# Kernel tuning notes

Hardware: AMD Instinct MI355X
Metric: run time of the kernel (lower is better)

## Reference

```python
import jax, jax.numpy as jnp
import numpy as np

D_MODEL = 1024
N_LAYER = 2
VOCAB = 50257
D_STATE = 64
D_CONV = 4
EXPAND = 2
HEADDIM = 64
D_INNER = EXPAND * D_MODEL            # 2048
NHEADS = D_INNER // HEADDIM           # 32
CONV_DIM = D_INNER + 2 * D_STATE      # x, B, C share the conv (ngroups=1)
D_PROJ = 2 * D_INNER + 2 * D_STATE + NHEADS  # z, xBC, dt
D_FF = 4 * D_MODEL
B, T = 1, 1024
EPS = 1e-5


def _layernorm(x, w):
    mu = jnp.mean(x, -1, keepdims=True)
    v = jnp.mean((x - mu) ** 2, -1, keepdims=True)
    return (x - mu) * jax.lax.rsqrt(v + EPS) * w


def _rmsnorm(x, w):
    return x * jax.lax.rsqrt(jnp.mean(x ** 2, -1, keepdims=True) + EPS) * w


def setup_inputs() -> dict:
    key = jax.random.key(0)
    ks = jax.random.split(key, 16)
    std = 0.02
    idx = jax.random.randint(ks[0], (B, T), 0, VOCAB)
    targets = jax.random.randint(ks[1], (B, T), 0, VOCAB)
    E = jax.random.normal(ks[2], (VOCAB, D_MODEL)) * std  # tied embedding / lm_head
    norm_w = jnp.ones((N_LAYER, D_MODEL))
    norm2_w = jnp.ones((N_LAYER, D_MODEL))
    norm_f_w = jnp.ones((D_MODEL,))
    in_proj_w = jax.random.normal(ks[3], (N_LAYER, D_PROJ, D_MODEL)) * std
    conv_w = jax.random.normal(ks[4], (N_LAYER, CONV_DIM, D_CONV)) / np.sqrt(D_CONV)
    conv_b = jnp.zeros((N_LAYER, CONV_DIM))
    dt = jnp.exp(jax.random.uniform(ks[5], (N_LAYER, NHEADS)) * (np.log(0.1) - np.log(1e-3)) + np.log(1e-3))
    dt_bias = dt + jnp.log(-jnp.expm1(-dt))  # inverse softplus
    A_log = jnp.log(jax.random.uniform(ks[6], (N_LAYER, NHEADS), minval=1.0, maxval=16.0))
    Dp = jnp.ones((N_LAYER, NHEADS))
    gnorm_w = jnp.ones((N_LAYER, D_INNER))
    out_proj_w = jax.random.normal(ks[7], (N_LAYER, D_MODEL, D_INNER)) * std / np.sqrt(2 * N_LAYER)
    fc1_w = jax.random.normal(ks[8], (N_LAYER, 2 * D_FF, D_MODEL)) * std
    fc2_w = jax.random.normal(ks[9], (N_LAYER, D_MODEL, D_FF)) * std / np.sqrt(2 * N_LAYER)
    return {"idx": idx, "targets": targets, "E": E, "norm_w": norm_w, "norm2_w": norm2_w,
            "in_proj_w": in_proj_w, "conv_w": conv_w, "conv_b": conv_b, "dt_bias": dt_bias,
            "A_log": A_log, "Dp": Dp, "gnorm_w": gnorm_w, "out_proj_w": out_proj_w,
            "fc1_w": fc1_w, "fc2_w": fc2_w, "norm_f_w": norm_f_w}


def _mamba2(x, Wi, cw, cb, dtb, Al, Dh, gw, Wo):
    b, l, _ = x.shape
    zxbcdt = x @ Wi.T  # [b,l,D_PROJ]
    z = zxbcdt[..., :D_INNER]
    xBC = zxbcdt[..., D_INNER:D_INNER + CONV_DIM]
    dt = zxbcdt[..., D_INNER + CONV_DIM:]  # [b,l,H]
    # depthwise causal conv1d over time
    xp = jnp.pad(xBC, ((0, 0), (D_CONV - 1, 0), (0, 0)))
    xBC = sum(xp[:, k:k + l, :] * cw[:, k] for k in range(D_CONV)) + cb
    xBC = jax.nn.silu(xBC)
    xs = xBC[..., :D_INNER].reshape(b, l, NHEADS, HEADDIM)
    Bm = xBC[..., D_INNER:D_INNER + D_STATE]  # [b,l,N] (ngroups=1)
    Cm = xBC[..., D_INNER + D_STATE:]
    dt = jax.nn.softplus(dt + dtb)            # [b,l,H]
    dA = jnp.exp(dt * (-jnp.exp(Al)))         # [b,l,H]
    tm = lambda a: jnp.moveaxis(a, 1, 0)      # time-major for scan

    def step(h, inp):
        dA_t, dt_t, x_t, B_t, C_t = inp
        h = dA_t[..., None, None] * h + jnp.einsum('bh,bhp,bn->bhpn', dt_t, x_t, B_t)
        return h, jnp.einsum('bhpn,bn->bhp', h, C_t)

    h0 = jnp.zeros((b, NHEADS, HEADDIM, D_STATE), x.dtype)
    _, ys = jax.lax.scan(step, h0, (tm(dA), tm(dt), tm(xs), tm(Bm), tm(Cm)))
    y = jnp.moveaxis(ys, 0, 1) + Dh[None, None, :, None] * xs  # skip term D*x
    y = y.reshape(b, l, D_INNER)
    y = _rmsnorm(y * jax.nn.silu(z), gw)  # gated RMSNorm
    return y @ Wo.T


def _gated_mlp(x, W1, W2):
    y = x @ W1.T
    y, g = jnp.split(y, 2, axis=-1)
    return (y * jax.nn.silu(g)) @ W2.T


def reference(idx, targets, E, norm_w, norm2_w, in_proj_w, conv_w, conv_b, dt_bias,
              A_log, Dp, gnorm_w, out_proj_w, fc1_w, fc2_w, norm_f_w):
    h = E[idx]  # [B,T,D]
    for i in range(N_LAYER):
        x = _layernorm(h, norm_w[i])
        x = _mamba2(x, in_proj_w[i], conv_w[i], conv_b[i], dt_bias[i], A_log[i],
                    Dp[i], gnorm_w[i], out_proj_w[i])
        res = x + h
        x = _layernorm(res, norm2_w[i])
        h = _gated_mlp(x, fc1_w[i], fc2_w[i]) + res
    h = _layernorm(h, norm_f_w)
    logits = h @ E.T  # tied lm_head
    logp = jax.nn.log_softmax(logits, axis=-1)
    nll = -jnp.take_along_axis(logp, targets[..., None], axis=-1)[..., 0]
    loss = jnp.mean(nll)  # no ignore_index=-1 entries present
    return logits, loss
```

## Files before the change

### kernel.cpp

```cpp
#include <hip/hip_runtime.h>
#include <cmath>

#define DMODEL  1024
#define DINNER  2048
#define NHEADS  32
#define CONVDIM 2176
#define DPROJ   4256
#define VOCAB   50257
#define NBLK_V  400
#define VOCABP  (NBLK_V * 128)
#define CLEN    16
#define NCHUNK  64

typedef float f32x4 __attribute__((ext_vector_type(4)));
typedef float f32x2 __attribute__((ext_vector_type(2)));
typedef unsigned short u16;
typedef u16 u16x4 __attribute__((ext_vector_type(4)));
typedef u16 u16x8 __attribute__((ext_vector_type(8)));
typedef __bf16 bf16x8 __attribute__((ext_vector_type(8)));

__device__ __forceinline__ u16 f2bf(float f) {
  unsigned u = __builtin_bit_cast(unsigned, f);
  u += 0x7FFFu + ((u >> 16) & 1u);
  return (u16)(u >> 16);
}
__device__ __forceinline__ float silu_f(float x) { return x / (1.f + expf(-x)); }

__device__ __forceinline__ void gload16(const u16* g, u16* l) {
  __builtin_amdgcn_global_load_lds(
      (const __attribute__((address_space(1))) void*)g,
      (__attribute__((address_space(3))) void*)l,
      16, 0, 0);
}

__global__ __launch_bounds__(256) void gemm_bf16(
    const u16* __restrict__ A, const u16* __restrict__ B,
    float* __restrict__ C, int N, int K, int kslice,
    float* __restrict__ lsepart, int swz, int nblk)
{
  __shared__ alignas(128) u16 As[128 * 64];
  __shared__ alignas(128) u16 Bs[128 * 64];
  const int tid = threadIdx.x;
  int m0, n0;
  if (swz) {
    int bid = blockIdx.x;
    m0 = ((bid >> 3) & 7) << 7;
    n0 = ((bid & 7) + ((bid >> 6) << 3)) << 7;
  } else {
    m0 = blockIdx.x << 7;
    n0 = blockIdx.y << 7;
  }
  const int lane = tid & 63, wid = tid >> 6;
  const int wm = (wid >> 1) << 6, wn = (wid & 1) << 6;
  const int lr = lane & 15, kg = lane >> 4;

  const int srow = wid * 8 + (lane >> 3);
  const int scol = ((lane & 7) ^ (lane >> 3)) << 3;
  const u16* gA = A + (size_t)(m0 + srow) * K + scol;
  const u16* gB = B + (size_t)(n0 + srow) * K + scol;

  f32x4 acc[4][4];
#pragma unroll
  for (int i = 0; i < 4; ++i)
#pragma unroll
    for (int j = 0; j < 4; ++j) acc[i][j] = (f32x4){0.f, 0.f, 0.f, 0.f};

  const int kb = blockIdx.z * kslice;
  const int ke = kb + kslice;
  for (int k0 = kb; k0 < ke; k0 += 64) {
#pragma unroll
    for (int i = 0; i < 4; ++i) {
      gload16(gA + k0 + (size_t)i * 32 * K, As + i * 2048 + wid * 512);
      gload16(gB + k0 + (size_t)i * 32 * K, Bs + i * 2048 + wid * 512);
    }
    __syncthreads();
#pragma unroll
    for (int kk = 0; kk < 2; ++kk) {
      bf16x8 af[4], bfr[4];
      const int cx = ((kk * 4 + kg) ^ (lr & 7)) << 3;
#pragma unroll
      for (int f = 0; f < 4; ++f) {
        af[f]  = *(const bf16x8*)&As[(wm + f * 16 + lr) * 64 + cx];
        bfr[f] = *(const bf16x8*)&Bs[(wn + f * 16 + lr) * 64 + cx];
      }
#pragma unroll
      for (int i = 0; i < 4; ++i)
#pragma unroll
        for (int j = 0; j < 4; ++j)
          acc[i][j] = __builtin_amdgcn_mfma_f32_16x16x32_bf16(af[i], bfr[j], acc[i][j], 0, 0, 0);
    }
    __syncthreads();
  }

  const int mr = (lane >> 4) << 2;
  const int nc = lane & 15;
  float* Cw = C + (gridDim.z > 1 ? (size_t)blockIdx.z * 1024 * N : 0);
#pragma unroll
  for (int i = 0; i < 4; ++i)
#pragma unroll
    for (int j = 0; j < 4; ++j) {
      int n = n0 + wn + j * 16 + nc;
      if (n < N) {
#pragma unroll
        for (int e = 0; e < 4; ++e)
          Cw[(size_t)(m0 + wm + i * 16 + mr + e) * N + n] = acc[i][j][e];
      }
    }

  if (lsepart) {
    float* Ls = (float*)As;
#pragma unroll
    for (int i = 0; i < 4; ++i)
#pragma unroll
      for (int e = 0; e < 4; ++e) {
        float pm = -1e30f;
#pragma unroll
        for (int j = 0; j < 4; ++j) {
          int n = n0 + wn + j * 16 + nc;
          if (n < N) pm = fmaxf(pm, acc[i][j][e]);
        }
        float ps = 0.f;
#pragma unroll
        for (int j = 0; j < 4; ++j) {
          int n = n0 + wn + j * 16 + nc;
          if (n < N) ps += expf(acc[i][j][e] - pm);
        }
#pragma unroll
        for (int o = 1; o < 16; o <<= 1) {
          float pm2 = __shfl_xor(pm, o), ps2 = __shfl_xor(ps, o);
          float M = fmaxf(pm, pm2);
          ps = ps * expf(pm - M) + ps2 * expf(pm2 - M);
          pm = M;
        }
        if (nc == 0) {
          int row = wm + i * 16 + mr + e;
          Ls[row * 4 + (wid & 1) * 2] = pm;
          Ls[row * 4 + (wid & 1) * 2 + 1] = ps;
        }
      }
    __syncthreads();
    if (tid < 128) {
      float pa = Ls[tid * 4], sa = Ls[tid * 4 + 1];
      float pb = Ls[tid * 4 + 2], sb = Ls[tid * 4 + 3];
      float M = fmaxf(pa, pb);
      float S = sa * expf(pa - M) + sb * expf(pb - M);
      ((f32x2*)lsepart)[(size_t)(m0 + tid) * nblk + (n0 >> 7)] = (f32x2){M, S};
    }
  }
}

__global__ void k_cvt8(const float* __restrict__ src, u16* __restrict__ dst, int n8) {
  int i = blockIdx.x * 256 + threadIdx.x;
  if (i >= n8) return;
  f32x4 a = ((const f32x4*)src)[i * 2];
  f32x4 b = ((const f32x4*)src)[i * 2 + 1];
  u16x8 o = { f2bf(a[0]), f2bf(a[1]), f2bf(a[2]), f2bf(a[3]),
              f2bf(b[0]), f2bf(b[1]), f2bf(b[2]), f2bf(b[3]) };
  ((u16x8*)dst)[i] = o;
}

__global__ void k_cvt8_pad(const float* __restrict__ src, u16* __restrict__ dst,
                           int n8, int srcN8) {
  int i = blockIdx.x * 256 + threadIdx.x;
  if (i >= n8) return;
  u16x8 o;
  if (i < srcN8) {
    f32x4 a = ((const f32x4*)src)[i * 2];
    f32x4 b = ((const f32x4*)src)[i * 2 + 1];
    o = (u16x8){ f2bf(a[0]), f2bf(a[1]), f2bf(a[2]), f2bf(a[3]),
                 f2bf(b[0]), f2bf(b[1]), f2bf(b[2]), f2bf(b[3]) };
  } else {
    o = (u16x8){0, 0, 0, 0, 0, 0, 0, 0};
  }
  ((u16x8*)dst)[i] = o;
}

__device__ __forceinline__ void ln_write(f32x4 v, const float* __restrict__ w,
                                         u16* __restrict__ out, int t, int tid) {
  float s = v[0] + v[1] + v[2] + v[3];
  float sq = v[0]*v[0] + v[1]*v[1] + v[2]*v[2] + v[3]*v[3];
#pragma unroll
  for (int o = 32; o; o >>= 1) { s += __shfl_down(s, o); sq += __shfl_down(sq, o); }
  __shared__ float sb[4], qb[4];
  if ((tid & 63) == 0) { sb[tid >> 6] = s; qb[tid >> 6] = sq; }
  __syncthreads();
  s = sb[0] + sb[1] + sb[2] + sb[3];
  sq = qb[0] + qb[1] + qb[2] + qb[3];
  float mu = s * (1.f / 1024.f);
  float rstd = rsqrtf(sq * (1.f / 1024.f) - mu * mu + 1e-5f);
  u16x4 o;
#pragma unroll
  for (int e = 0; e < 4; ++e) o[e] = f2bf((v[e] - mu) * rstd * w[tid * 4 + e]);
  ((u16x4*)out)[t * 256 + tid] = o;
}

__global__ void k_ln_embed(const int* __restrict__ idx, const float* __restrict__ E,
                           const float* __restrict__ w, float* __restrict__ hbuf,
                           u16* __restrict__ out) {
  int t = blockIdx.x, tid = threadIdx.x;
  f32x4 v = ((const f32x4*)(E + (size_t)idx[t] * DMODEL))[tid];
  ((f32x4*)hbuf)[t * 256 + tid] = v;
  ln_write(v, w, out, t, tid);
}

__global__ void k_red_ln(const float* __restrict__ part, int S,
                         float* __restrict__ hbuf, const float* __restrict__ w,
                         u16* __restrict__ out) {
  int t = blockIdx.x, tid = threadIdx.x;
  f32x4 v = ((const f32x4*)hbuf)[t * 256 + tid];
  for (int k = 0; k < S; ++k)
    v += ((const f32x4*)part)[(size_t)k * 262144 + t * 256 + tid];
  ((f32x4*)hbuf)[t * 256 + tid] = v;
  ln_write(v, w, out, t, tid);
}

__global__ void k_convdt(const float* __restrict__ zx, const float* __restrict__ cw,
                         const float* __restrict__ cb, const float* __restrict__ dtb,
                         const float* __restrict__ alog, float* __restrict__ xbc,
                         float* __restrict__ dtsp, float* __restrict__ dag) {
  int t = blockIdx.y, x = blockIdx.x, tid = threadIdx.x;
  if (x < 8 || tid < 128) {
    int c = x * 256 + tid;
    float acc = cb[c];
#pragma unroll
    for (int k = 0; k < 4; ++k) {
      int tt = t + k - 3;
      if (tt >= 0) acc += zx[(size_t)tt * DPROJ + 2048 + c] * cw[c * 4 + k];
    }
    xbc[(size_t)t * CONVDIM + c] = silu_f(acc);
  } else if (tid < 160) {
    int hh = tid - 128;
    float raw = zx[(size_t)t * DPROJ + 4224 + hh] + dtb[hh];
    float sp = raw > 20.f ? raw : log1pf(expf(raw));
    dtsp[t * 32 + hh] = sp;
    dag[t * 32 + hh] = expf(-expf(alog[hh]) * sp);
  }
}

__global__ void k_prefix(const float* __restrict__ dag, float* __restrict__ pref,
                         float* __restrict__ dacum) {
  int gi = blockIdx.x * 256 + threadIdx.x;
  int c = gi >> 5, hh = gi & 31;
  float P = 1.f;
  for (int s_ = 0; s_ < CLEN; ++s_) {
    int t = c * CLEN + s_;
    P *= dag[t * 32 + hh];
    pref[t * 32 + hh] = P;
  }
  dacum[gi] = P;
}

__global__ __launch_bounds__(256) void k_scan_local(
    const float* __restrict__ xbc, const float* __restrict__ dtsp,
    const float* __restrict__ dag, float* __restrict__ yb, float* __restrict__ Sloc)
{
  int c = blockIdx.x, hh = blockIdx.y;
  int tid = threadIdx.x;
  int p = tid >> 2, ng = tid & 3, n0 = ng << 4;
  float st[16];
#pragma unroll
  for (int j = 0; j < 16; ++j) st[j] = 0.f;
  for (int s_ = 0; s_ < CLEN; ++s_) {
    int t = c * CLEN + s_;
    float dA = dag[t * 32 + hh];
    float coef = dtsp[t * 32 + hh] * xbc[(size_t)t * CONVDIM + hh * 64 + p];
    const f32x4* B4 = (const f32x4*)&xbc[(size_t)t * CONVDIM + 2048 + n0];
    const f32x4* C4 = (const f32x4*)&xbc[(size_t)t * CONVDIM + 2112 + n0];
    float y = 0.f;
#pragma unroll
    for (int q = 0; q < 4; ++q) {
      f32x4 b = B4[q], cc = C4[q];
#pragma unroll
      for (int e = 0; e < 4; ++e) {
        int j = q * 4 + e;
        st[j] = dA * st[j] + coef * b[e];
        y += st[j] * cc[e];
      }
    }
    y += __shfl_xor(y, 1);
    y += __shfl_xor(y, 2);
    if (ng == 0) yb[(size_t)t * DINNER + hh * 64 + p] = y;
  }
  float* Sp = Sloc + ((size_t)(c * 32 + hh) * 64 + p) * 64 + n0;
#pragma unroll
  for (int q = 0; q < 4; ++q)
    *(f32x4*)(Sp + q * 4) = (f32x4){ st[q*4], st[q*4+1], st[q*4+2], st[q*4+3] };
}

__global__ void k_chain(const float* __restrict__ Sloc, const float* __restrict__ dacum,
                        float* __restrict__ Sin) {
  int e = blockIdx.x * 256 + threadIdx.x;
  int hh = e >> 12;
  float S = 0.f;
  for (int c = 0; c < NCHUNK; ++c) {
    Sin[(size_t)c * 131072 + e] = S;
    S = dacum[c * 32 + hh] * S + Sloc[(size_t)c * 131072 + e];
  }
}

__global__ __launch_bounds__(256) void k_scan_fix(
    const float* __restrict__ xbc, const float* __restrict__ pref,
    const float* __restrict__ Sin, const float* __restrict__ Dp,
    float* __restrict__ yb)
{
  __shared__ float Sl[64 * 68];
  int c = blockIdx.x, hh = blockIdx.y;
  int tid = threadIdx.x;
  for (int i = 0; i < 16; ++i) {
    int e = i * 256 + tid;
    Sl[(e >> 6) * 68 + (e & 63)] = Sin[(size_t)(c * 32 + hh) * 4096 + e];
  }
  __syncthreads();
  int p = tid >> 2, ng = tid & 3, n0 = ng << 4;
  float Dh = Dp[hh];
  for (int s_ = 0; s_ < CLEN; ++s_) {
    int t = c * CLEN + s_;
    const f32x4* C4 = (const f32x4*)&xbc[(size_t)t * CONVDIM + 2112 + n0];
    float yc = 0.f;
#pragma unroll
    for (int q = 0; q < 4; ++q) {
      f32x4 cc = C4[q];
#pragma unroll
      for (int e = 0; e < 4; ++e) yc += Sl[p * 68 + n0 + q * 4 + e] * cc[e];
    }
    yc += __shfl_xor(yc, 1);
    yc += __shfl_xor(yc, 2);
    if (ng == 0) {
      size_t oy = (size_t)t * DINNER + hh * 64 + p;
      yb[oy] = yb[oy] + pref[t * 32 + hh] * yc + Dh * xbc[(size_t)t * CONVDIM + hh * 64 + p];
    }
  }
}

__global__ void k_gated_rms(const float* __restrict__ yb, const float* __restrict__ zx,
                            const float* __restrict__ gw, u16* __restrict__ out) {
  int t = blockIdx.x, tid = threadIdx.x;
  float v[8], ss = 0.f;
#pragma unroll
  for (int i = 0; i < 8; ++i) {
    int j = tid + i * 256;
    float z = zx[(size_t)t * DPROJ + j];
    float vv = yb[(size_t)t * DINNER + j] * silu_f(z);
    v[i] = vv; ss += vv * vv;
  }
#pragma unroll
  for (int o = 32; o; o >>= 1) ss += __shfl_down(ss, o);
  __shared__ float sb[4];
  if ((tid & 63) == 0) sb[tid >> 6] = ss;
  __syncthreads();
  ss = sb[0] + sb[1] + sb[2] + sb[3];
  float rstd = rsqrtf(ss * (1.f / 2048.f) + 1e-5f);
#pragma unroll
  for (int i = 0; i < 8; ++i) {
    int j = tid + i * 256;
    out[(size_t)t * DINNER + j] = f2bf(v[i] * rstd * gw[j]);
  }
}

__global__ void k_glu(const float* __restrict__ fc1, u16* __restrict__ out) {
  int gi = blockIdx.x * 256 + threadIdx.x;
  int t = gi >> 12, j = gi & 4095;
  float y = fc1[(size_t)t * 8192 + j];
  float g = fc1[(size_t)t * 8192 + 4096 + j];
  out[gi] = f2bf(y * silu_f(g));
}

__global__ void k_loss_final(const float* __restrict__ lsepart,
                             const float* __restrict__ logits,
                             const int* __restrict__ tgt, float* __restrict__ part) {
  int t = blockIdx.x, tid = threadIdx.x;
  float m = -1e30f, s = 0.f;
  for (int nb = tid; nb < NBLK_V; nb += 256) {
    f32x2 v = ((const f32x2*)lsepart)[(size_t)t * NBLK_V + nb];
    float M = fmaxf(m, v[0]);
    s = s * expf(m - M) + v[1] * expf(v[0] - M);
    m = M;
  }
#pragma unroll
  for (int o = 32; o; o >>= 1) {
    float m2 = __shfl_down(m, o), s2 = __shfl_down(s, o);
    float M = fmaxf(m, m2);
    s = s * expf(m - M) + s2 * expf(m2 - M);
    m = M;
  }
  __shared__ float ms[4], ssh[4];
  if ((tid & 63) == 0) { ms[tid >> 6] = m; ssh[tid >> 6] = s; }
  __syncthreads();
  if (tid == 0) {
    float M = ms[0], S = ssh[0];
    for (int w = 1; w < 4; ++w) {
      float M2 = fmaxf(M, ms[w]);
      S = S * expf(M - M2) + ssh[w] * expf(ms[w] - M2);
      M = M2;
    }
    part[t] = (M + logf(S)) - logits[(size_t)t * VOCAB + tgt[t]];
  }
}

__global__ void k_loss_mean(const float* __restrict__ part, float* __restrict__ out) {
  int tid = threadIdx.x;
  float s = 0.f;
  for (int j = tid; j < 1024; j += 256) s += part[j];
#pragma unroll
  for (int o = 32; o; o >>= 1) s += __shfl_down(s, o);
  __shared__ float sb[4];
  if ((tid & 63) == 0) sb[tid >> 6] = s;
  __syncthreads();
  if (tid == 0) out[0] = (sb[0] + sb[1] + sb[2] + sb[3]) * (1.f / 1024.f);
}

extern "C" void kernel_launch(void* const* d_in, const int* in_sizes, int n_in,
                              void* d_out, int out_size, void* d_ws, size_t ws_size,
                              hipStream_t stream)
{
  const int*   idx       = (const int*)d_in[0];
  const int*   tgt       = (const int*)d_in[1];
  const float* E         = (const float*)d_in[2];
  const float* norm_w    = (const float*)d_in[3];
  const float* norm2_w   = (const float*)d_in[4];
  const float* in_proj_w = (const float*)d_in[5];
  const float* conv_w    = (const float*)d_in[6];
  const float* conv_b    = (const float*)d_in[7];
  const float* dt_bias   = (const float*)d_in[8];
  const float* A_log     = (const float*)d_in[9];
  const float* Dp        = (const float*)d_in[10];
  const float* gnorm_w   = (const float*)d_in[11];
  const float* out_proj_w= (const float*)d_in[12];
  const float* fc1_w     = (const float*)d_in[13];
  const float* fc2_w     = (const float*)d_in[14];
  const float* norm_f_w  = (const float*)d_in[15];
  float* logits = (float*)d_out;
  (void)in_sizes; (void)n_in; (void)out_size; (void)ws_size;

  char* W = (char*)d_ws;
  size_t off = 0;
  auto A8 = [&](size_t bytes) { void* p = W + off; off = (off + bytes + 255) & ~(size_t)255; return p; };
  float* hbuf   = (float*)A8((size_t)1024 * 1024 * 4);
  u16*   xnormb = (u16*)  A8((size_t)1024 * 1024 * 2);
  u16*   gatedb = (u16*)  A8((size_t)1024 * 2048 * 2);
  u16*   glub   = (u16*)  A8((size_t)1024 * 4096 * 2);
  float* dtsp   = (float*)A8((size_t)1024 * 32 * 4);
  float* dag    = (float*)A8((size_t)1024 * 32 * 4);
  float* pref   = (float*)A8((size_t)1024 * 32 * 4);
  float* dacum  = (float*)A8((size_t)2048 * 4);
  float* lpart  = (float*)A8((size_t)1024 * 4);
  float* lsebuf = (float*)A8((size_t)1024 * NBLK_V * 2 * 4);
  u16*   wip    = (u16*)  A8((size_t)2 * 4352 * 1024 * 2);
  u16*   wop    = (u16*)  A8((size_t)2 * 1024 * 2048 * 2);
  u16*   wfc1   = (u16*)  A8((size_t)2 * 8192 * 1024 * 2);
  u16*   wfc2   = (u16*)  A8((size_t)2 * 1024 * 4096 * 2);
  char*  span   = (char*)A8((size_t)117964800);
  float* big0   = (float*)(span);
  float* xbc    = (float*)(span + 33554432);
  float* yb     = (float*)(span + 33554432 + 8912896);
  float* Sloc   = (float*)(span + 33554432 + 8912896 + 8388608);
  float* Sin    = (float*)((char*)Sloc + 33554432);
  float* part   = Sloc;
  u16*   Ebf    = (u16*)span;

  dim3 b256(256);

  k_cvt8_pad<<<dim3((4352*1024/8 + 255)/256), b256, 0, stream>>>(
      in_proj_w, wip, 4352*1024/8, 4256*1024/8);
  k_cvt8_pad<<<dim3((4352*1024/8 + 255)/256), b256, 0, stream>>>(
      in_proj_w + (size_t)4256*1024, wip + (size_t)4352*1024, 4352*1024/8, 4256*1024/8);
  k_cvt8<<<dim3(2*1024*2048/8/256), b256, 0, stream>>>(out_proj_w, wop, 2*1024*2048/8);
  k_cvt8<<<dim3(2*8192*1024/8/256), b256, 0, stream>>>(fc1_w, wfc1, 2*8192*1024/8);
  k_cvt8<<<dim3(2*1024*4096/8/256), b256, 0, stream>>>(fc2_w, wfc2, 2*1024*4096/8);

  k_ln_embed<<<1024, b256, 0, stream>>>(idx, E, norm_w, hbuf, xnormb);

  const float* nw_next[2] = { norm_w + 1024, norm_f_w };
  for (int L = 0; L < 2; ++L) {
    gemm_bf16<<<dim3(8, 34, 1), b256, 0, stream>>>(
        xnormb, wip + (size_t)L * 4352 * 1024, big0, DPROJ, 1024, 1024, nullptr, 0, 34);
    k_convdt<<<dim3(9, 1024), b256, 0, stream>>>(
        big0, conv_w + L * CONVDIM * 4, conv_b + L * CONVDIM,
        dt_bias + L * 32, A_log + L * 32, xbc, dtsp, dag);
    k_prefix<<<8, b256, 0, stream>>>(dag, pref, dacum);
    k_scan_local<<<dim3(64, 32), b256, 0, stream>>>(xbc, dtsp, dag, yb, Sloc);
    k_chain<<<512, b256, 0, stream>>>(Sloc, dacum, Sin);
    k_scan_fix<<<dim3(64, 32), b256, 0, stream>>>(xbc, pref, Sin, Dp + L * 32, yb);
    k_gated_rms<<<1024, b256, 0, stream>>>(yb, big0, gnorm_w + L * 2048, gatedb);
    gemm_bf16<<<dim3(8, 8, 2), b256, 0, stream>>>(
        gatedb, wop + (size_t)L * 1024 * 2048, part, 1024, 2048, 1024, nullptr, 0, 8);
    k_red_ln<<<1024, b256, 0, stream>>>(part, 2, hbuf, norm2_w + L * 1024, xnormb);
    gemm_bf16<<<dim3(8, 64, 1), b256, 0, stream>>>(
        xnormb, wfc1 + (size_t)L * 8192 * 1024, big0, 8192, 1024, 1024, nullptr, 0, 64);
    k_glu<<<16384, b256, 0, stream>>>(big0, glub);
    gemm_bf16<<<dim3(8, 8, 4), b256, 0, stream>>>(
        glub, wfc2 + (size_t)L * 1024 * 4096, part, 1024, 4096, 1024, nullptr, 0, 8);
    k_red_ln<<<1024, b256, 0, stream>>>(part, 4, hbuf, nw_next[L], xnormb);
  }

  k_cvt8_pad<<<dim3((VOCABP*1024/8 + 255)/256), b256, 0, stream>>>(
      E, Ebf, VOCABP*1024/8, VOCAB*1024/8);
  gemm_bf16<<<dim3(8 * NBLK_V, 1, 1), b256, 0, stream>>>(
      xnormb, Ebf, logits, VOCAB, 1024, 1024, lsebuf, 1, NBLK_V);
  k_loss_final<<<1024, b256, 0, stream>>>(lsebuf, logits, tgt, lpart);
  k_loss_mean<<<1, b256, 0, stream>>>(lpart, logits + (size_t)1024 * VOCAB);
}
```

Baseline: 899.7 us.

## Double-buffer GEMM LDS, fuse GLU into fc1 GEMM, fold prefix into scan

The GEMM kernel now uses two LDS buffers so the global-to-LDS loads for the next K tile are issued while MFMAs run on the current one. The fc1 weights are interleaved at conversion time so the value and gate columns sit next to each other, which lets the fc1 GEMM epilogue apply silu gating and write bf16 directly. That removes the fp32 fc1 output round-trip and the separate GLU kernel. The prefix-product kernel is folded into the local scan, and the LSE epilogue is simplified to a max reduction followed by a sum. The cost is doubled LDS (64KB per block), which may reduce occupancy.

```diff
diff --git a/kernel.cpp b/kernel.cpp
--- a/kernel.cpp
+++ b/kernel.cpp
@@ -36,10 +36,11 @@
 __global__ __launch_bounds__(256) void gemm_bf16(
     const u16* __restrict__ A, const u16* __restrict__ B,
     float* __restrict__ C, int N, int K, int kslice,
-    float* __restrict__ lsepart, int swz, int nblk)
+    float* __restrict__ lsepart, int swz, int nblk,
+    u16* __restrict__ glu_out)
 {
-  __shared__ alignas(128) u16 As[128 * 64];
-  __shared__ alignas(128) u16 Bs[128 * 64];
+  __shared__ alignas(128) u16 As[2][128 * 64];
+  __shared__ alignas(128) u16 Bs[2][128 * 64];
   const int tid = threadIdx.x;
   int m0, n0;
   if (swz) {
@@ -66,22 +67,31 @@
     for (int j = 0; j < 4; ++j) acc[i][j] = (f32x4){0.f, 0.f, 0.f, 0.f};
 
   const int kb = blockIdx.z * kslice;
-  const int ke = kb + kslice;
-  for (int k0 = kb; k0 < ke; k0 += 64) {
+  const int nt = kslice >> 6;
+
+  auto stage = [&](int buf, int kk) {
 #pragma unroll
     for (int i = 0; i < 4; ++i) {
-      gload16(gA + k0 + (size_t)i * 32 * K, As + i * 2048 + wid * 512);
-      gload16(gB + k0 + (size_t)i * 32 * K, Bs + i * 2048 + wid * 512);
-    }
-    __syncthreads();
+      gload16(gA + kk + (size_t)i * 32 * K, &As[buf][i * 2048 + wid * 512]);
+      gload16(gB + kk + (size_t)i * 32 * K, &Bs[buf][i * 2048 + wid * 512]);
+    }
+  };
+
+  stage(0, kb);
+  asm volatile("s_waitcnt vmcnt(0)" ::: "memory");
+  __builtin_amdgcn_s_barrier();
+
+  int cur = 0;
+  for (int t = 0; t < nt; ++t) {
+    if (t + 1 < nt) stage(cur ^ 1, kb + (t + 1) * 64);
 #pragma unroll
     for (int kk = 0; kk < 2; ++kk) {
       bf16x8 af[4], bfr[4];
       const int cx = ((kk * 4 + kg) ^ (lr & 7)) << 3;
 #pragma unroll
       for (int f = 0; f < 4; ++f) {
-        af[f]  = *(const bf16x8*)&As[(wm + f * 16 + lr) * 64 + cx];
-        bfr[f] = *(const bf16x8*)&Bs[(wn + f * 16 + lr) * 64 + cx];
+        af[f]  = *(const bf16x8*)&As[cur][(wm + f * 16 + lr) * 64 + cx];
+        bfr[f] = *(const bf16x8*)&Bs[cur][(wn + f * 16 + lr) * 64 + cx];
       }
 #pragma unroll
       for (int i = 0; i < 4; ++i)
@@ -89,11 +99,32 @@
         for (int j = 0; j < 4; ++j)
           acc[i][j] = __builtin_amdgcn_mfma_f32_16x16x32_bf16(af[i], bfr[j], acc[i][j], 0, 0, 0);
     }
-    __syncthreads();
+    asm volatile("s_waitcnt vmcnt(0)" ::: "memory");
+    __builtin_amdgcn_s_barrier();
+    cur ^= 1;
   }
 
   const int mr = (lane >> 4) << 2;
   const int nc = lane & 15;
+
+  if (glu_out) {
+#pragma unroll
+    for (int i = 0; i < 4; ++i)
+#pragma unroll
+      for (int j = 0; j < 4; ++j)
+#pragma unroll
+        for (int e = 0; e < 4; ++e) {
+          float v = acc[i][j][e];
+          float p = __shfl_xor(v, 1);
+          if (!(nc & 1)) {
+            int q = (n0 + wn + j * 16 + nc) >> 1;
+            int row = m0 + wm + i * 16 + mr + e;
+            glu_out[(size_t)row * 4096 + q] = f2bf(v * silu_f(p));
+          }
+        }
+    return;
+  }
+
   float* Cw = C + (gridDim.z > 1 ? (size_t)blockIdx.z * 1024 * N : 0);
 #pragma unroll
   for (int i = 0; i < 4; ++i)
@@ -119,6 +150,8 @@
           int n = n0 + wn + j * 16 + nc;
           if (n < N) pm = fmaxf(pm, acc[i][j][e]);
         }
+#pragma unroll
+        for (int o = 1; o < 16; o <<= 1) pm = fmaxf(pm, __shfl_xor(pm, o));
         float ps = 0.f;
 #pragma unroll
         for (int j = 0; j < 4; ++j) {
@@ -126,12 +159,7 @@
           if (n < N) ps += expf(acc[i][j][e] - pm);
         }
 #pragma unroll
-        for (int o = 1; o < 16; o <<= 1) {
-          float pm2 = __shfl_xor(pm, o), ps2 = __shfl_xor(ps, o);
-          float M = fmaxf(pm, pm2);
-          ps = ps * expf(pm - M) + ps2 * expf(pm2 - M);
-          pm = M;
-        }
+        for (int o = 1; o < 16; o <<= 1) ps += __shfl_xor(ps, o);
         if (nc == 0) {
           int row = wm + i * 16 + mr + e;
           Ls[row * 4 + (wid & 1) * 2] = pm;
@@ -175,6 +203,19 @@
   ((u16x8*)dst)[i] = o;
 }
 
+__global__ void k_cvt_fc1(const float* __restrict__ src, u16* __restrict__ dst, int n8) {
+  int i = blockIdx.x * 256 + threadIdx.x;
+  if (i >= n8) return;
+  f32x4 a = ((const f32x4*)src)[i * 2];
+  f32x4 b = ((const f32x4*)src)[i * 2 + 1];
+  u16x8 o = { f2bf(a[0]), f2bf(a[1]), f2bf(a[2]), f2bf(a[3]),
+              f2bf(b[0]), f2bf(b[1]), f2bf(b[2]), f2bf(b[3]) };
+  int R = i >> 7, col8 = i & 127;
+  int layer = R >> 13, r = R & 8191;
+  int dstr = (r < 4096) ? (r << 1) : (((r - 4096) << 1) | 1);
+  ((u16x8*)dst)[((size_t)(layer << 13) + dstr) * 128 + col8] = o;
+}
+
 __device__ __forceinline__ void ln_write(f32x4 v, const float* __restrict__ w,
                                          u16* __restrict__ out, int t, int tid) {
   float s = v[0] + v[1] + v[2] + v[3];
@@ -237,22 +278,10 @@
   }
 }
 
-__global__ void k_prefix(const float* __restrict__ dag, float* __restrict__ pref,
-                         float* __restrict__ dacum) {
-  int gi = blockIdx.x * 256 + threadIdx.x;
-  int c = gi >> 5, hh = gi & 31;
-  float P = 1.f;
-  for (int s_ = 0; s_ < CLEN; ++s_) {
-    int t = c * CLEN + s_;
-    P *= dag[t * 32 + hh];
-    pref[t * 32 + hh] = P;
-  }
-  dacum[gi] = P;
-}
-
 __global__ __launch_bounds__(256) void k_scan_local(
     const float* __restrict__ xbc, const float* __restrict__ dtsp,
-    const float* __restrict__ dag, float* __restrict__ yb, float* __restrict__ Sloc)
+    const float* __restrict__ dag, float* __restrict__ yb, float* __restrict__ Sloc,
+    float* __restrict__ pref, float* __restrict__ dacum)
 {
   int c = blockIdx.x, hh = blockIdx.y;
   int tid = threadIdx.x;
@@ -260,9 +289,12 @@
   float st[16];
 #pragma unroll
   for (int j = 0; j < 16; ++j) st[j] = 0.f;
+  float P = 1.f;
   for (int s_ = 0; s_ < CLEN; ++s_) {
     int t = c * CLEN + s_;
     float dA = dag[t * 32 + hh];
+    P *= dA;
+    if (tid == 0) pref[t * 32 + hh] = P;
     float coef = dtsp[t * 32 + hh] * xbc[(size_t)t * CONVDIM + hh * 64 + p];
     const f32x4* B4 = (const f32x4*)&xbc[(size_t)t * CONVDIM + 2048 + n0];
     const f32x4* C4 = (const f32x4*)&xbc[(size_t)t * CONVDIM + 2112 + n0];
@@ -281,6 +313,7 @@
     y += __shfl_xor(y, 2);
     if (ng == 0) yb[(size_t)t * DINNER + hh * 64 + p] = y;
   }
+  if (tid == 0) dacum[c * 32 + hh] = P;
   float* Sp = Sloc + ((size_t)(c * 32 + hh) * 64 + p) * 64 + n0;
 #pragma unroll
   for (int q = 0; q < 4; ++q)
@@ -355,14 +388,6 @@
     int j = tid + i * 256;
     out[(size_t)t * DINNER + j] = f2bf(v[i] * rstd * gw[j]);
   }
-}
-
-__global__ void k_glu(const float* __restrict__ fc1, u16* __restrict__ out) {
-  int gi = blockIdx.x * 256 + threadIdx.x;
-  int t = gi >> 12, j = gi & 4095;
-  float y = fc1[(size_t)t * 8192 + j];
-  float g = fc1[(size_t)t * 8192 + 4096 + j];
-  out[gi] = f2bf(y * silu_f(g));
 }
 
 __global__ void k_loss_final(const float* __restrict__ lsepart,
@@ -465,7 +490,7 @@
   k_cvt8_pad<<<dim3((4352*1024/8 + 255)/256), b256, 0, stream>>>(
       in_proj_w + (size_t)4256*1024, wip + (size_t)4352*1024, 4352*1024/8, 4256*1024/8);
   k_cvt8<<<dim3(2*1024*2048/8/256), b256, 0, stream>>>(out_proj_w, wop, 2*1024*2048/8);
-  k_cvt8<<<dim3(2*8192*1024/8/256), b256, 0, stream>>>(fc1_w, wfc1, 2*8192*1024/8);
+  k_cvt_fc1<<<dim3(2*8192*1024/8/256), b256, 0, stream>>>(fc1_w, wfc1, 2*8192*1024/8);
   k_cvt8<<<dim3(2*1024*4096/8/256), b256, 0, stream>>>(fc2_w, wfc2, 2*1024*4096/8);
 
   k_ln_embed<<<1024, b256, 0, stream>>>(idx, E, norm_w, hbuf, xnormb);
@@ -473,30 +498,32 @@
   const float* nw_next[2] = { norm_w + 1024, norm_f_w };
   for (int L = 0; L < 2; ++L) {
     gemm_bf16<<<dim3(8, 34, 1), b256, 0, stream>>>(
-        xnormb, wip + (size_t)L * 4352 * 1024, big0, DPROJ, 1024, 1024, nullptr, 0, 34);
+        xnormb, wip + (size_t)L * 4352 * 1024, big0, DPROJ, 1024, 1024,
+        nullptr, 0, 34, nullptr);
     k_convdt<<<dim3(9, 1024), b256, 0, stream>>>(
         big0, conv_w + L * CONVDIM * 4, conv_b + L * CONVDIM,
         dt_bias + L * 32, A_log + L * 32, xbc, dtsp, dag);
-    k_prefix<<<8, b256, 0, stream>>>(dag, pref, dacum);
-    k_scan_local<<<dim3(64, 32), b256, 0, stream>>>(xbc, dtsp, dag, yb, Sloc);
+    k_scan_local<<<dim3(64, 32), b256, 0, stream>>>(xbc, dtsp, dag, yb, Sloc, pref, dacum);
     k_chain<<<512, b256, 0, stream>>>(Sloc, dacum, Sin);
     k_scan_fix<<<dim3(64, 32), b256, 0, stream>>>(xbc, pref, Sin, Dp + L * 32, yb);
     k_gated_rms<<<1024, b256, 0, stream>>>(yb, big0, gnorm_w + L * 2048, gatedb);
     gemm_bf16<<<dim3(8, 8, 2), b256, 0, stream>>>(
-        gatedb, wop + (size_t)L * 1024 * 2048, part, 1024, 2048, 1024, nullptr, 0, 8);
+        gatedb, wop + (size_t)L * 1024 * 2048, part, 1024, 2048, 1024,
+        nullptr, 0, 8, nullptr);
     k_red_ln<<<1024, b256, 0, stream>>>(part, 2, hbuf, norm2_w + L * 1024, xnormb);
     gemm_bf16<<<dim3(8, 64, 1), b256, 0, stream>>>(
-        xnormb, wfc1 + (size_t)L * 8192 * 1024, big0, 8192, 1024, 1024, nullptr, 0, 64);
-    k_glu<<<16384, b256, 0, stream>>>(big0, glub);
+        xnormb, wfc1 + (size_t)L * 8192 * 1024, nullptr, 8192, 1024, 1024,
+        nullptr, 0, 64, glub);
     gemm_bf16<<<dim3(8, 8, 4), b256, 0, stream>>>(
-        glub, wfc2 + (size_t)L * 1024 * 4096, part, 1024, 4096, 1024, nullptr, 0, 8);
+        glub, wfc2 + (size_t)L * 1024 * 4096, part, 1024, 4096, 1024,
+        nullptr, 0, 8, nullptr);
     k_red_ln<<<1024, b256, 0, stream>>>(part, 4, hbuf, nw_next[L], xnormb);
   }
 
   k_cvt8_pad<<<dim3((VOCABP*1024/8 + 255)/256), b256, 0, stream>>>(
       E, Ebf, VOCABP*1024/8, VOCAB*1024/8);
   gemm_bf16<<<dim3(8 * NBLK_V, 1, 1), b256, 0, stream>>>(
-      xnormb, Ebf, logits, VOCAB, 1024, 1024, lsebuf, 1, NBLK_V);
+      xnormb, Ebf, logits, VOCAB, 1024, 1024, lsebuf, 1, NBLK_V, nullptr);
   k_loss_final<<<1024, b256, 0, stream>>>(lsebuf, logits, tgt, lpart);
   k_loss_mean<<<1, b256, 0, stream>>>(lpart, logits + (size_t)1024 * VOCAB);
 }
```

Result: faster. 837.2 us (-6.9%).
